# Kernel optimization log

Hardware: AMD Instinct MI355X
Metric: run time of the kernel (lower is better)

## Reference

```python
import jax, jax.numpy as jnp
import numpy as np

HEAD_DIM = 64
NUM_HEADS = 32
ROPE_THETA = 10000.0


def _rope_cos_sin(seq_len, dim, theta, dtype):
    inv_freq = 1.0 / (theta ** (jnp.arange(0, dim, 2, dtype=jnp.float32) / dim))
    t = jnp.arange(seq_len, dtype=jnp.float32)
    freqs = jnp.outer(t, inv_freq)  # [T, dim/2]
    return jnp.cos(freqs).astype(dtype), jnp.sin(freqs).astype(dtype)


def _apply_rope(x, cos, sin):
    # x: [B, T, H, D]; GPT-NeoX style (split halves), matching flash-attn rotary (interleaved=False)
    d2 = x.shape[-1] // 2
    x1, x2 = x[..., :d2], x[..., d2:]
    c = cos[None, :, None, :]
    s = sin[None, :, None, :]
    return jnp.concatenate([x1 * c - x2 * s, x2 * c + x1 * s], axis=-1)


def setup_inputs() -> dict:
    key = jax.random.key(0)
    ks = jax.random.split(key, 8)
    B, T, Dm = 2, 2048, 2048
    H, Dh = NUM_HEADS, HEAD_DIM
    sc = 1.0 / np.sqrt(Dm)
    return {
        "hidden_states": jax.random.normal(ks[0], (B, T, Dm), jnp.float32),
        "v1": jax.random.normal(ks[1], (B, T, H, Dh), jnp.float32),
        "lambda1": jax.random.uniform(ks[2], (), jnp.float32),
        "Wq": jax.random.normal(ks[3], (Dm, Dm), jnp.float32) * sc,
        "Wk": jax.random.normal(ks[4], (Dm, Dm), jnp.float32) * sc,
        "Wv": jax.random.normal(ks[5], (Dm, Dm), jnp.float32) * sc,
        "Wo": jax.random.normal(ks[6], (Dm, Dm), jnp.float32) * sc,
        "lambda2": jnp.float32(0.5),
    }


def reference(hidden_states, v1, lambda1, Wq, Wk, Wv, Wo, lambda2):
    B, T, Dm = hidden_states.shape
    H, Dh = NUM_HEADS, HEAD_DIM
    # QKV projections + head split
    q = (hidden_states @ Wq).reshape(B, T, H, Dh)
    k = (hidden_states @ Wk).reshape(B, T, H, Dh)
    v = (hidden_states @ Wv).reshape(B, T, H, Dh)
    # Value residual mixing: V' = lambda1 * V_1 + lambda2 * V_n
    v = lambda1 * v1 + lambda2 * v
    # RoPE (seqlen_offset = 0, no cache)
    cos, sin = _rope_cos_sin(T, Dh, ROPE_THETA, q.dtype)
    q = _apply_rope(q, cos, sin)
    k = _apply_rope(k, cos, sin)
    # Causal attention (flash_attn_func(..., causal=True) equivalent)
    scale = 1.0 / np.sqrt(Dh)
    scores = jnp.einsum("bqhd,bkhd->bhqk", q, k) * scale
    causal = jnp.tril(jnp.ones((T, T), dtype=bool))
    scores = jnp.where(causal[None, None], scores, jnp.finfo(scores.dtype).min)
    probs = jax.nn.softmax(scores, axis=-1)
    o = jnp.einsum("bhqk,bkhd->bqhd", probs, v).reshape(B, T, Dm)
    return o @ Wo
```

## Files before the change

### kernel.cpp

```cpp
#include <hip/hip_runtime.h>
#include <hip/hip_bf16.h>
#include <math.h>

typedef __bf16 bf16;
typedef __bf16 bf16x8 __attribute__((ext_vector_type(8)));
typedef __bf16 bf16x4 __attribute__((ext_vector_type(4)));
typedef float  f32x4  __attribute__((ext_vector_type(4)));
typedef short  sv4    __attribute__((ext_vector_type(4)));

#define B_  2
#define T_  2048
#define DM  2048
#define H_  32
#define DH  64

__device__ __forceinline__ bf16x8 load8(const bf16* p) {
    return *reinterpret_cast<const bf16x8*>(p);
}

__device__ __forceinline__ void gld16(const bf16* g, bf16* l) {
    __builtin_amdgcn_global_load_lds(
        (const __attribute__((address_space(1))) unsigned int*)g,
        (__attribute__((address_space(3))) unsigned int*)l, 16, 0, 0);
}

__global__ void k_convert(const float* __restrict__ in, bf16* __restrict__ out, int n4) {
    int i = blockIdx.x * blockDim.x + threadIdx.x;
    if (i < n4) {
        float4 v = reinterpret_cast<const float4*>(in)[i];
        bf16x4 o;
        o[0] = (bf16)v.x; o[1] = (bf16)v.y; o[2] = (bf16)v.z; o[3] = (bf16)v.w;
        reinterpret_cast<bf16x4*>(out)[i] = o;
    }
}

__global__ void k_transposeW(const float* __restrict__ Wq, const float* __restrict__ Wk,
                             const float* __restrict__ Wv, const float* __restrict__ Wo,
                             bf16* __restrict__ WqT, bf16* __restrict__ WkT,
                             bf16* __restrict__ WvT, bf16* __restrict__ WoT) {
    const float* in; bf16* out;
    switch (blockIdx.z) {
        case 0: in = Wq; out = WqT; break;
        case 1: in = Wk; out = WkT; break;
        case 2: in = Wv; out = WvT; break;
        default: in = Wo; out = WoT; break;
    }
    __shared__ float tile[32][33];
    int tx = threadIdx.x, ty = threadIdx.y;
    int x0 = blockIdx.x * 32, y0 = blockIdx.y * 32;
    #pragma unroll
    for (int i = 0; i < 4; i++)
        tile[ty + i*8][tx] = in[(size_t)(y0 + ty + i*8) * DM + x0 + tx];
    __syncthreads();
    #pragma unroll
    for (int i = 0; i < 4; i++)
        out[(size_t)(x0 + ty + i*8) * DM + y0 + tx] = (bf16)tile[tx][ty + i*8];
}

template<int OUT_BF16>
__global__ __launch_bounds__(256)
void k_gemm(const bf16* __restrict__ A, const bf16* __restrict__ BT,
            void* __restrict__ Cout, int ldc) {
    constexpr int K = 2048;
    __shared__ bf16 ldsA[128 * 32];
    __shared__ bf16 ldsB[128 * 32];
    int tid = threadIdx.x;
    int lane = tid & 63, w = tid >> 6;
    int l16 = lane & 15, quad = lane >> 4;
    int wm = w >> 1, wn = w & 1;
    int mblk = blockIdx.y * 128, nblk = blockIdx.x * 128;

    f32x4 acc[4][4] = {};

    const bf16* gA = A  + (size_t)(mblk + w * 32 + (lane >> 2)) * K + (lane & 3) * 8;
    const bf16* gB = BT + (size_t)(nblk + w * 32 + (lane >> 2)) * K + (lane & 3) * 8;
    bf16* lA = ldsA + w * 1024;
    bf16* lB = ldsB + w * 1024;

    for (int k0 = 0; k0 < K; k0 += 32) {
        gld16(gA + k0,          lA);
        gld16(gA + 16 * K + k0, lA + 512);
        gld16(gB + k0,          lB);
        gld16(gB + 16 * K + k0, lB + 512);
        __syncthreads();
        bf16x8 af[4], bfr[4];
        #pragma unroll
        for (int s = 0; s < 4; s++)
            af[s] = *reinterpret_cast<bf16x8*>(&ldsA[(wm * 64 + s * 16 + l16) * 32 + quad * 8]);
        #pragma unroll
        for (int t = 0; t < 4; t++)
            bfr[t] = *reinterpret_cast<bf16x8*>(&ldsB[(wn * 64 + t * 16 + l16) * 32 + quad * 8]);
        #pragma unroll
        for (int s = 0; s < 4; s++)
            #pragma unroll
            for (int t = 0; t < 4; t++)
                acc[s][t] = __builtin_amdgcn_mfma_f32_16x16x32_bf16(af[s], bfr[t], acc[s][t], 0, 0, 0);
        __syncthreads();
    }

    #pragma unroll
    for (int s = 0; s < 4; s++) {
        int row = mblk + wm * 64 + s * 16 + quad * 4;
        #pragma unroll
        for (int t = 0; t < 4; t++) {
            int col = nblk + wn * 64 + t * 16 + l16;
            #pragma unroll
            for (int r = 0; r < 4; r++) {
                if (OUT_BF16)
                    reinterpret_cast<bf16*>(Cout)[(size_t)(row + r) * ldc + col] = (bf16)acc[s][t][r];
                else
                    reinterpret_cast<float*>(Cout)[(size_t)(row + r) * ldc + col] = acc[s][t][r];
            }
        }
    }
}

__global__ void k_rope(bf16* __restrict__ qkv) {
    int id = blockIdx.x * 256 + threadIdx.x;
    int i = id & 31;
    int h = (id >> 5) & 31;
    int t = (id >> 10) & 2047;
    int b = (id >> 21) & 1;
    int sel = id >> 22;
    size_t base = ((size_t)(b * T_ + t)) * 6144 + sel * 2048 + h * 64;
    float inv = expf(-(float)i * (9.210340371976184f / 32.0f));
    float ang = (float)t * inv;
    float s, c;
    sincosf(ang, &s, &c);
    float x1 = (float)qkv[base + i];
    float x2 = (float)qkv[base + i + 32];
    qkv[base + i]      = (bf16)(x1 * c - x2 * s);
    qkv[base + i + 32] = (bf16)(x2 * c + x1 * s);
}

__global__ void k_combinev(const float* __restrict__ v1, const bf16* __restrict__ qkv,
                           const float* __restrict__ l1p, const float* __restrict__ l2p,
                           bf16* __restrict__ vT) {
    __shared__ float tile[64 * 33];
    float l1 = l1p[0], l2 = l2p[0];
    int b = blockIdx.y >> 5, h = blockIdx.y & 31;
    int t0 = blockIdx.x * 32;
    int tid = threadIdx.x;
    int d = tid & 63, tr = tid >> 6;
    #pragma unroll
    for (int i = 0; i < 8; i++) {
        int t = t0 + i * 4 + tr;
        size_t iv1 = ((size_t)(b * T_ + t)) * 2048 + h * 64 + d;
        size_t ivg = ((size_t)(b * T_ + t)) * 6144 + 4096 + h * 64 + d;
        tile[d * 33 + i * 4 + tr] = l1 * v1[iv1] + l2 * (float)qkv[ivg];
    }
    __syncthreads();
    int tl = tid & 31, dr = tid >> 5;
    #pragma unroll
    for (int j = 0; j < 8; j++) {
        int d2 = dr + j * 8;
        vT[((size_t)((b * H_ + h) * 64 + d2)) * T_ + t0 + tl] = (bf16)tile[d2 * 33 + tl];
    }
}

__global__ __launch_bounds__(256)
void k_attn(const bf16* __restrict__ qkv, const bf16* __restrict__ vT, bf16* __restrict__ o) {
    __shared__ bf16 ldsK[64 * 72];
    __shared__ bf16 ldsV[64 * 68];
    int bx = blockIdx.x;
    int bh = blockIdx.y;
    int b = bh >> 5, h = bh & 31;
    int tid = threadIdx.x;
    int lane = tid & 63, w = tid >> 6;
    int l16 = lane & 15, quad = lane >> 4;

    int srow = tid >> 3, sseg = tid & 7;
    const bf16* kg = qkv + (size_t)(b * T_) * 6144 + 2048 + h * 64 + sseg * 8;
    const bf16* vg = vT + (size_t)bh * DH * T_ + sseg * 8;

    #pragma unroll 1
    for (int pass = 0; pass < 2; pass++) {
        int qt = pass ? (15 - bx) : bx;
        int qbase = qt * 128 + w * 32;

        bf16x8 qf[2][2];
        #pragma unroll
        for (int qs = 0; qs < 2; qs++) {
            size_t qrow = (size_t)(b * T_ + qbase + qs * 16 + l16) * 6144 + h * 64;
            #pragma unroll
            for (int half = 0; half < 2; half++) {
                bf16x8 v = load8(qkv + qrow + half * 32 + quad * 8);
                #pragma unroll
                for (int e = 0; e < 8; e++) v[e] = (bf16)((float)v[e] * 0.1803368801f);
                qf[qs][half] = v;
            }
        }

        f32x4 accO[2][4] = {};
        float m_[2] = {-1e30f, -1e30f};
        float pl[2] = {0.f, 0.f};

        int nkt = 2 * qt + 2;
        for (int kt = 0; kt < nkt; kt++) {
            int key0 = kt * 64;
            #pragma unroll
            for (int j = 0; j < 2; j++) {
                int row = j * 32 + srow;
                *reinterpret_cast<uint4*>(&ldsK[row * 72 + sseg * 8]) =
                    *reinterpret_cast<const uint4*>(kg + (size_t)(key0 + row) * 6144);
                *reinterpret_cast<uint4*>(&ldsV[row * 68 + sseg * 8]) =
                    *reinterpret_cast<const uint4*>(vg + (size_t)row * T_ + key0);
            }
            __syncthreads();

            f32x4 st[2][4];
            #pragma unroll
            for (int ks = 0; ks < 4; ks++) {
                bf16x8 kf0 = *reinterpret_cast<bf16x8*>(&ldsK[(ks * 16 + l16) * 72 + quad * 8]);
                bf16x8 kf1 = *reinterpret_cast<bf16x8*>(&ldsK[(ks * 16 + l16) * 72 + 32 + quad * 8]);
                #pragma unroll
                for (int qs = 0; qs < 2; qs++) {
                    f32x4 z = {};
                    z = __builtin_amdgcn_mfma_f32_16x16x32_bf16(kf0, qf[qs][0], z, 0, 0, 0);
                    z = __builtin_amdgcn_mfma_f32_16x16x32_bf16(kf1, qf[qs][1], z, 0, 0, 0);
                    st[qs][ks] = z;
                }
            }

            sv4 pk[2][4];
            #pragma unroll
            for (int qs = 0; qs < 2; qs++) {
                int qcol = qbase + qs * 16 + l16;
                #pragma unroll
                for (int ks = 0; ks < 4; ks++) {
                    if (key0 + ks * 16 + 15 > qbase + qs * 16) {
                        #pragma unroll
                        for (int r = 0; r < 4; r++)
                            if (key0 + ks * 16 + quad * 4 + r > qcol) st[qs][ks][r] = -3e38f;
                    }
                }
                float mx = st[qs][0][0];
                #pragma unroll
                for (int ks = 0; ks < 4; ks++)
                    #pragma unroll
                    for (int r = 0; r < 4; r++) mx = fmaxf(mx, st[qs][ks][r]);
                mx = fmaxf(mx, __shfl_xor(mx, 16));
                mx = fmaxf(mx, __shfl_xor(mx, 32));
                if (__any(mx > m_[qs])) {
                    float nm = fmaxf(m_[qs], mx);
                    float alpha = __builtin_amdgcn_exp2f(m_[qs] - nm);
                    m_[qs] = nm;
                    pl[qs] *= alpha;
                    #pragma unroll
                    for (int n2 = 0; n2 < 4; n2++) accO[qs][n2] *= alpha;
                }
                float nm = m_[qs];
                float rsum = 0.f;
                #pragma unroll
                for (int ks = 0; ks < 4; ks++) {
                    bf16x4 ph;
                    #pragma unroll
                    for (int r = 0; r < 4; r++) {
                        float p = __builtin_amdgcn_exp2f(st[qs][ks][r] - nm);
                        rsum += p;
                        ph[r] = (bf16)p;
                    }
                    pk[qs][ks] = __builtin_bit_cast(sv4, ph);
                }
                pl[qs] += rsum;
            }

            #pragma unroll
            for (int ks = 0; ks < 4; ks++) {
                #pragma unroll
                for (int n2 = 0; n2 < 4; n2++) {
                    sv4 vf = *reinterpret_cast<sv4*>(&ldsV[(n2 * 16 + l16) * 68 + ks * 16 + quad * 4]);
                    #pragma unroll
                    for (int qs = 0; qs < 2; qs++)
                        accO[qs][n2] = __builtin_amdgcn_mfma_f32_16x16x16bf16_1k(
                            vf, pk[qs][ks], accO[qs][n2], 0, 0, 0);
                }
            }
            __syncthreads();
        }

        #pragma unroll
        for (int qs = 0; qs < 2; qs++) {
            float l = pl[qs];
            l += __shfl_xor(l, 16);
            l += __shfl_xor(l, 32);
            float inv = 1.0f / l;
            int query = qbase + qs * 16 + l16;
            #pragma unroll
            for (int n2 = 0; n2 < 4; n2++) {
                bf16x4 ov;
                #pragma unroll
                for (int r = 0; r < 4; r++) ov[r] = (bf16)(accO[qs][n2][r] * inv);
                *reinterpret_cast<bf16x4*>(
                    &o[(size_t)(b * T_ + query) * DM + h * 64 + n2 * 16 + quad * 4]) = ov;
            }
        }
    }
}

extern "C" void kernel_launch(void* const* d_in, const int* in_sizes, int n_in,
                              void* d_out, int out_size, void* d_ws, size_t ws_size,
                              hipStream_t stream) {
    const float* hs   = (const float*)d_in[0];
    const float* v1   = (const float*)d_in[1];
    const float* lam1 = (const float*)d_in[2];
    const float* Wq   = (const float*)d_in[3];
    const float* Wk   = (const float*)d_in[4];
    const float* Wv   = (const float*)d_in[5];
    const float* Wo   = (const float*)d_in[6];
    const float* lam2 = (const float*)d_in[7];

    char* ws = (char*)d_ws;
    bf16* hs_bf = (bf16*)(ws);
    bf16* Wcat  = (bf16*)(ws + 16777216);
    bf16* WoT   = (bf16*)(ws + 41943040);
    bf16* qkv   = (bf16*)(ws + 50331648);
    bf16* vT_bf = (bf16*)(ws + 100663296);
    bf16* o_bf  = (bf16*)(ws + 117440512);

    k_convert<<<8192, 256, 0, stream>>>(hs, hs_bf, 2097152);
    k_transposeW<<<dim3(64, 64, 4), dim3(32, 8), 0, stream>>>(
        Wq, Wk, Wv, Wo, Wcat, Wcat + 4194304, Wcat + 8388608, WoT);

    k_gemm<1><<<dim3(48, 32), 256, 0, stream>>>(hs_bf, Wcat, (void*)qkv, 6144);

    k_rope<<<32768, 256, 0, stream>>>(qkv);
    k_combinev<<<dim3(64, 64), 256, 0, stream>>>(v1, qkv, lam1, lam2, vT_bf);

    k_attn<<<dim3(8, 64), 256, 0, stream>>>(qkv, vT_bf, o_bf);

    k_gemm<0><<<dim3(16, 32), 256, 0, stream>>>(o_bf, WoT, d_out, 2048);
}
```

Before: 445.1 us.

## Fuse RoPE into QKV GEMM epilogue, swizzle LDS, retile attention to 64-row blocks

Removes the standalone RoPE kernel by applying the rotation in the QKV GEMM epilogue on the fp32 accumulators, using fast sincos. Adds an XOR swizzle to the GEMM and attention LDS layouts to avoid bank conflicts without padding. Switches attention K/V staging to direct global-to-LDS loads. Retiles attention to 64-query blocks with 16 rows per wave, doubling the grid and skipping fully masked diagonal subtiles. Fast sincos at large angles may reduce accuracy, and the smaller query tiles reuse each K/V tile less.

New measurement: 469.1 us. +5.4%, slower.

```diff
diff --git a/kernel.cpp b/kernel.cpp
--- a/kernel.cpp
+++ b/kernel.cpp
@@ -57,7 +57,7 @@
         out[(size_t)(x0 + ty + i*8) * DM + y0 + tx] = (bf16)tile[tx][ty + i*8];
 }
 
-template<int OUT_BF16>
+template<int OUT_BF16, int ROPE>
 __global__ __launch_bounds__(256)
 void k_gemm(const bf16* __restrict__ A, const bf16* __restrict__ BT,
             void* __restrict__ Cout, int ldc) {
@@ -72,10 +72,12 @@
 
     f32x4 acc[4][4] = {};
 
-    const bf16* gA = A  + (size_t)(mblk + w * 32 + (lane >> 2)) * K + (lane & 3) * 8;
-    const bf16* gB = BT + (size_t)(nblk + w * 32 + (lane >> 2)) * K + (lane & 3) * 8;
+    int sgz = ((lane & 3) ^ ((lane >> 3) & 3)) * 8;
+    const bf16* gA = A  + (size_t)(mblk + w * 32 + (lane >> 2)) * K + sgz;
+    const bf16* gB = BT + (size_t)(nblk + w * 32 + (lane >> 2)) * K + sgz;
     bf16* lA = ldsA + w * 1024;
     bf16* lB = ldsB + w * 1024;
+    int sA = (quad ^ ((l16 >> 1) & 3)) * 8;
 
     for (int k0 = 0; k0 < K; k0 += 32) {
         gld16(gA + k0,          lA);
@@ -86,16 +88,37 @@
         bf16x8 af[4], bfr[4];
         #pragma unroll
         for (int s = 0; s < 4; s++)
-            af[s] = *reinterpret_cast<bf16x8*>(&ldsA[(wm * 64 + s * 16 + l16) * 32 + quad * 8]);
+            af[s] = *reinterpret_cast<bf16x8*>(&ldsA[(wm * 64 + s * 16 + l16) * 32 + sA]);
         #pragma unroll
         for (int t = 0; t < 4; t++)
-            bfr[t] = *reinterpret_cast<bf16x8*>(&ldsB[(wn * 64 + t * 16 + l16) * 32 + quad * 8]);
+            bfr[t] = *reinterpret_cast<bf16x8*>(&ldsB[(wn * 64 + t * 16 + l16) * 32 + sA]);
         #pragma unroll
         for (int s = 0; s < 4; s++)
             #pragma unroll
             for (int t = 0; t < 4; t++)
                 acc[s][t] = __builtin_amdgcn_mfma_f32_16x16x32_bf16(af[s], bfr[t], acc[s][t], 0, 0, 0);
         __syncthreads();
+    }
+
+    if (ROPE && nblk < 4096) {
+        #pragma unroll
+        for (int t = 0; t < 2; t++) {
+            int dim = t * 16 + l16;
+            float invf = __builtin_amdgcn_exp2f(-(float)dim * 0.41524101186092037f);
+            #pragma unroll
+            for (int s = 0; s < 4; s++) {
+                #pragma unroll
+                for (int r = 0; r < 4; r++) {
+                    int row = mblk + wm * 64 + s * 16 + quad * 4 + r;
+                    float ang = (float)(row & 2047) * invf;
+                    float sn, cs;
+                    __sincosf(ang, &sn, &cs);
+                    float x1 = acc[s][t][r], x2 = acc[s][t + 2][r];
+                    acc[s][t][r]     = x1 * cs - x2 * sn;
+                    acc[s][t + 2][r] = x2 * cs + x1 * sn;
+                }
+            }
+        }
     }
 
     #pragma unroll
@@ -113,24 +136,6 @@
             }
         }
     }
-}
-
-__global__ void k_rope(bf16* __restrict__ qkv) {
-    int id = blockIdx.x * 256 + threadIdx.x;
-    int i = id & 31;
-    int h = (id >> 5) & 31;
-    int t = (id >> 10) & 2047;
-    int b = (id >> 21) & 1;
-    int sel = id >> 22;
-    size_t base = ((size_t)(b * T_ + t)) * 6144 + sel * 2048 + h * 64;
-    float inv = expf(-(float)i * (9.210340371976184f / 32.0f));
-    float ang = (float)t * inv;
-    float s, c;
-    sincosf(ang, &s, &c);
-    float x1 = (float)qkv[base + i];
-    float x2 = (float)qkv[base + i + 32];
-    qkv[base + i]      = (bf16)(x1 * c - x2 * s);
-    qkv[base + i + 32] = (bf16)(x2 * c + x1 * s);
 }
 
 __global__ void k_combinev(const float* __restrict__ v1, const bf16* __restrict__ qkv,
@@ -160,8 +165,8 @@
 
 __global__ __launch_bounds__(256)
 void k_attn(const bf16* __restrict__ qkv, const bf16* __restrict__ vT, bf16* __restrict__ o) {
-    __shared__ bf16 ldsK[64 * 72];
-    __shared__ bf16 ldsV[64 * 68];
+    __shared__ bf16 ldsK[64 * 64];
+    __shared__ bf16 ldsV[64 * 64];
     int bx = blockIdx.x;
     int bh = blockIdx.y;
     int b = bh >> 5, h = bh & 31;
@@ -169,131 +174,125 @@
     int lane = tid & 63, w = tid >> 6;
     int l16 = lane & 15, quad = lane >> 4;
 
-    int srow = tid >> 3, sseg = tid & 7;
-    const bf16* kg = qkv + (size_t)(b * T_) * 6144 + 2048 + h * 64 + sseg * 8;
-    const bf16* vg = vT + (size_t)bh * DH * T_ + sseg * 8;
+    int rl = lane >> 3, sg = ((lane & 7) ^ rl) * 8;
+    const bf16* kgl = qkv + ((size_t)(b * T_) + w * 16 + rl) * 6144 + 2048 + h * 64 + sg;
+    const bf16* vgl = vT + ((size_t)bh * DH + w * 16 + rl) * T_ + sg;
+    bf16* lKw = ldsK + w * 16 * 64;
+    bf16* lVw = ldsV + w * 16 * 64;
+
+    int skey = (quad ^ (l16 & 7)) * 8;
+    int skey2 = ((quad + 4) ^ (l16 & 7)) * 8;
 
     #pragma unroll 1
     for (int pass = 0; pass < 2; pass++) {
-        int qt = pass ? (15 - bx) : bx;
-        int qbase = qt * 128 + w * 32;
-
-        bf16x8 qf[2][2];
-        #pragma unroll
-        for (int qs = 0; qs < 2; qs++) {
-            size_t qrow = (size_t)(b * T_ + qbase + qs * 16 + l16) * 6144 + h * 64;
-            #pragma unroll
-            for (int half = 0; half < 2; half++) {
-                bf16x8 v = load8(qkv + qrow + half * 32 + quad * 8);
-                #pragma unroll
-                for (int e = 0; e < 8; e++) v[e] = (bf16)((float)v[e] * 0.1803368801f);
-                qf[qs][half] = v;
-            }
-        }
-
-        f32x4 accO[2][4] = {};
-        float m_[2] = {-1e30f, -1e30f};
-        float pl[2] = {0.f, 0.f};
-
-        int nkt = 2 * qt + 2;
+        int qt = pass ? (31 - bx) : bx;
+        int qbase = qt * 64 + w * 16;
+
+        size_t qrow = (size_t)(b * T_ + qbase + l16) * 6144 + h * 64;
+        bf16x8 qf[2];
+        #pragma unroll
+        for (int half = 0; half < 2; half++) {
+            bf16x8 v = load8(qkv + qrow + half * 32 + quad * 8);
+            #pragma unroll
+            for (int e = 0; e < 8; e++) v[e] = (bf16)((float)v[e] * 0.1803368801f);
+            qf[half] = v;
+        }
+
+        f32x4 accO[4] = {};
+        float m_ = -1e30f, pl = 0.f;
+
+        int nkt = qt + 1;
         for (int kt = 0; kt < nkt; kt++) {
             int key0 = kt * 64;
             #pragma unroll
             for (int j = 0; j < 2; j++) {
-                int row = j * 32 + srow;
-                *reinterpret_cast<uint4*>(&ldsK[row * 72 + sseg * 8]) =
-                    *reinterpret_cast<const uint4*>(kg + (size_t)(key0 + row) * 6144);
-                *reinterpret_cast<uint4*>(&ldsV[row * 68 + sseg * 8]) =
-                    *reinterpret_cast<const uint4*>(vg + (size_t)row * T_ + key0);
+                gld16(kgl + (size_t)(key0 + j * 8) * 6144, lKw + j * 512);
+                gld16(vgl + (size_t)(j * 8) * T_ + key0,   lVw + j * 512);
             }
             __syncthreads();
 
-            f32x4 st[2][4];
+            bool diag = (kt == qt);
+            f32x4 st[4];
+            sv4 pk[4];
             #pragma unroll
             for (int ks = 0; ks < 4; ks++) {
-                bf16x8 kf0 = *reinterpret_cast<bf16x8*>(&ldsK[(ks * 16 + l16) * 72 + quad * 8]);
-                bf16x8 kf1 = *reinterpret_cast<bf16x8*>(&ldsK[(ks * 16 + l16) * 72 + 32 + quad * 8]);
-                #pragma unroll
-                for (int qs = 0; qs < 2; qs++) {
+                if (!diag || key0 + ks * 16 <= qbase + 15) {
+                    bf16x8 kf0 = *reinterpret_cast<bf16x8*>(&ldsK[(ks * 16 + l16) * 64 + skey]);
+                    bf16x8 kf1 = *reinterpret_cast<bf16x8*>(&ldsK[(ks * 16 + l16) * 64 + skey2]);
                     f32x4 z = {};
-                    z = __builtin_amdgcn_mfma_f32_16x16x32_bf16(kf0, qf[qs][0], z, 0, 0, 0);
-                    z = __builtin_amdgcn_mfma_f32_16x16x32_bf16(kf1, qf[qs][1], z, 0, 0, 0);
-                    st[qs][ks] = z;
+                    z = __builtin_amdgcn_mfma_f32_16x16x32_bf16(kf0, qf[0], z, 0, 0, 0);
+                    z = __builtin_amdgcn_mfma_f32_16x16x32_bf16(kf1, qf[1], z, 0, 0, 0);
+                    st[ks] = z;
+                } else {
+                    st[ks] = (f32x4){-3e38f, -3e38f, -3e38f, -3e38f};
                 }
             }
 
-            sv4 pk[2][4];
-            #pragma unroll
-            for (int qs = 0; qs < 2; qs++) {
-                int qcol = qbase + qs * 16 + l16;
-                #pragma unroll
-                for (int ks = 0; ks < 4; ks++) {
-                    if (key0 + ks * 16 + 15 > qbase + qs * 16) {
-                        #pragma unroll
-                        for (int r = 0; r < 4; r++)
-                            if (key0 + ks * 16 + quad * 4 + r > qcol) st[qs][ks][r] = -3e38f;
+            if (diag) {
+                int qcol = qbase + l16;
+                #pragma unroll
+                for (int ks = 0; ks < 4; ks++)
+                    #pragma unroll
+                    for (int r = 0; r < 4; r++)
+                        if (key0 + ks * 16 + quad * 4 + r > qcol) st[ks][r] = -3e38f;
+            }
+
+            float mx = st[0][0];
+            #pragma unroll
+            for (int ks = 0; ks < 4; ks++)
+                #pragma unroll
+                for (int r = 0; r < 4; r++) mx = fmaxf(mx, st[ks][r]);
+            mx = fmaxf(mx, __shfl_xor(mx, 16));
+            mx = fmaxf(mx, __shfl_xor(mx, 32));
+            if (__any(mx > m_)) {
+                float nm = fmaxf(m_, mx);
+                float alpha = __builtin_amdgcn_exp2f(m_ - nm);
+                m_ = nm;
+                pl *= alpha;
+                #pragma unroll
+                for (int n2 = 0; n2 < 4; n2++) accO[n2] *= alpha;
+            }
+            float rsum = 0.f;
+            #pragma unroll
+            for (int ks = 0; ks < 4; ks++) {
+                bf16x4 ph;
+                #pragma unroll
+                for (int r = 0; r < 4; r++) {
+                    float p = __builtin_amdgcn_exp2f(st[ks][r] - m_);
+                    rsum += p;
+                    ph[r] = (bf16)p;
+                }
+                pk[ks] = __builtin_bit_cast(sv4, ph);
+            }
+            pl += rsum;
+
+            #pragma unroll
+            for (int ks = 0; ks < 4; ks++) {
+                if (!diag || key0 + ks * 16 <= qbase + 15) {
+                    int svf = ((ks * 2 + (quad >> 1)) ^ (l16 & 7)) * 8 + (quad & 1) * 4;
+                    #pragma unroll
+                    for (int n2 = 0; n2 < 4; n2++) {
+                        sv4 vf = *reinterpret_cast<sv4*>(&ldsV[(n2 * 16 + l16) * 64 + svf]);
+                        accO[n2] = __builtin_amdgcn_mfma_f32_16x16x16bf16_1k(
+                            vf, pk[ks], accO[n2], 0, 0, 0);
                     }
                 }
-                float mx = st[qs][0][0];
-                #pragma unroll
-                for (int ks = 0; ks < 4; ks++)
-                    #pragma unroll
-                    for (int r = 0; r < 4; r++) mx = fmaxf(mx, st[qs][ks][r]);
-                mx = fmaxf(mx, __shfl_xor(mx, 16));
-                mx = fmaxf(mx, __shfl_xor(mx, 32));
-                if (__any(mx > m_[qs])) {
-                    float nm = fmaxf(m_[qs], mx);
-                    float alpha = __builtin_amdgcn_exp2f(m_[qs] - nm);
-                    m_[qs] = nm;
-                    pl[qs] *= alpha;
-                    #pragma unroll
-                    for (int n2 = 0; n2 < 4; n2++) accO[qs][n2] *= alpha;
-                }
-                float nm = m_[qs];
-                float rsum = 0.f;
-                #pragma unroll
-                for (int ks = 0; ks < 4; ks++) {
-                    bf16x4 ph;
-                    #pragma unroll
-                    for (int r = 0; r < 4; r++) {
-                        float p = __builtin_amdgcn_exp2f(st[qs][ks][r] - nm);
-                        rsum += p;
-                        ph[r] = (bf16)p;
-                    }
-                    pk[qs][ks] = __builtin_bit_cast(sv4, ph);
-                }
-                pl[qs] += rsum;
-            }
-
-            #pragma unroll
-            for (int ks = 0; ks < 4; ks++) {
-                #pragma unroll
-                for (int n2 = 0; n2 < 4; n2++) {
-                    sv4 vf = *reinterpret_cast<sv4*>(&ldsV[(n2 * 16 + l16) * 68 + ks * 16 + quad * 4]);
-                    #pragma unroll
-                    for (int qs = 0; qs < 2; qs++)
-                        accO[qs][n2] = __builtin_amdgcn_mfma_f32_16x16x16bf16_1k(
-                            vf, pk[qs][ks], accO[qs][n2], 0, 0, 0);
-                }
             }
             __syncthreads();
         }
 
-        #pragma unroll
-        for (int qs = 0; qs < 2; qs++) {
-            float l = pl[qs];
-            l += __shfl_xor(l, 16);
-            l += __shfl_xor(l, 32);
-            float inv = 1.0f / l;
-            int query = qbase + qs * 16 + l16;
-            #pragma unroll
-            for (int n2 = 0; n2 < 4; n2++) {
-                bf16x4 ov;
-                #pragma unroll
-                for (int r = 0; r < 4; r++) ov[r] = (bf16)(accO[qs][n2][r] * inv);
-                *reinterpret_cast<bf16x4*>(
-                    &o[(size_t)(b * T_ + query) * DM + h * 64 + n2 * 16 + quad * 4]) = ov;
-            }
+        float l = pl;
+        l += __shfl_xor(l, 16);
+        l += __shfl_xor(l, 32);
+        float inv = 1.0f / l;
+        int query = qbase + l16;
+        #pragma unroll
+        for (int n2 = 0; n2 < 4; n2++) {
+            bf16x4 ov;
+            #pragma unroll
+            for (int r = 0; r < 4; r++) ov[r] = (bf16)(accO[n2][r] * inv);
+            *reinterpret_cast<bf16x4*>(
+                &o[(size_t)(b * T_ + query) * DM + h * 64 + n2 * 16 + quad * 4]) = ov;
         }
     }
 }
@@ -322,12 +321,11 @@
     k_transposeW<<<dim3(64, 64, 4), dim3(32, 8), 0, stream>>>(
         Wq, Wk, Wv, Wo, Wcat, Wcat + 4194304, Wcat + 8388608, WoT);
 
-    k_gemm<1><<<dim3(48, 32), 256, 0, stream>>>(hs_bf, Wcat, (void*)qkv, 6144);
-
-    k_rope<<<32768, 256, 0, stream>>>(qkv);
+    k_gemm<1, 1><<<dim3(48, 32), 256, 0, stream>>>(hs_bf, Wcat, (void*)qkv, 6144);
+
     k_combinev<<<dim3(64, 64), 256, 0, stream>>>(v1, qkv, lam1, lam2, vT_bf);
 
-    k_attn<<<dim3(8, 64), 256, 0, stream>>>(qkv, vT_bf, o_bf);
-
-    k_gemm<0><<<dim3(16, 32), 256, 0, stream>>>(o_bf, WoT, d_out, 2048);
-}
+    k_attn<<<dim3(16, 64), 256, 0, stream>>>(qkv, vT_bf, o_bf);
+
+    k_gemm<0, 0><<<dim3(16, 32), 256, 0, stream>>>(o_bf, WoT, d_out, 2048);
+}
```
